# Optimization experiments

Measured on AMD Instinct MI355X. Metric: run time of the kernel, lower is better.

The kernel has to match this reference:

```python
import jax, jax.numpy as jnp
import numpy as np

B, R, F = 64, 196, 2048   # batch, regions, feature_dim
E, H, A = 512, 512, 512   # embed_dim, hidden_dim, attn_dim
V, L = 12000, 24          # vocab, seq_len


def setup_inputs() -> dict:
    key = jax.random.key(0)
    ks = jax.random.split(key, 16)
    s = lambda *d: 1.0 / np.sqrt(d[-1])
    inp = {
        'image_feats': jax.random.normal(ks[0], (B, R, F), jnp.float32),
        'caption_in': jax.random.randint(ks[1], (B, L), 0, V, jnp.int64),
        'emb_table': jax.random.normal(ks[2], (V, E), jnp.float32) * 0.02,
        'W_init_h': jax.random.normal(ks[3], (H, F), jnp.float32) * s(F),
        'b_init_h': jnp.zeros((H,), jnp.float32),
        'W_init_c': jax.random.normal(ks[4], (H, F), jnp.float32) * s(F),
        'b_init_c': jnp.zeros((H,), jnp.float32),
        'W_ih': jax.random.normal(ks[5], (4 * H, E + F), jnp.float32) * s(E + F),
        'b_ih': jnp.zeros((4 * H,), jnp.float32),
        'W_hh': jax.random.normal(ks[6], (4 * H, H), jnp.float32) * s(H),
        'b_hh': jnp.zeros((4 * H,), jnp.float32),
        'W_featp': jax.random.normal(ks[7], (A, F), jnp.float32) * s(F),
        'b_featp': jnp.zeros((A,), jnp.float32),
        'W_hidp': jax.random.normal(ks[8], (A, H), jnp.float32) * s(H),
        'b_hidp': jnp.zeros((A,), jnp.float32),
        'W_score': jax.random.normal(ks[9], (1, A), jnp.float32) * s(A),
        'b_score': jnp.zeros((1,), jnp.float32),
        'W_out': jax.random.normal(ks[10], (V, H), jnp.float32) * s(H),
        'b_out': jnp.zeros((V,), jnp.float32),
    }
    return inp


def _forward(image_feats, caption_in, emb_table, W_init_h, b_init_h, W_init_c,
             b_init_c, W_ih, b_ih, W_hh, b_hh, W_featp, b_featp, W_hidp,
             b_hidp, W_score, b_score, W_out, b_out):
    # init hidden state from mean image features
    mean_feats = image_feats.mean(axis=1)                      # (B, F)
    h0 = mean_feats @ W_init_h.T + b_init_h                    # (B, H)
    c0 = mean_feats @ W_init_c.T + b_init_c                    # (B, H)

    embeddings = emb_table[caption_in]                         # (B, L, E)  (dropout in eval mode = identity)

    # feature projection is constant over timesteps -> hoist out of the scan
    feat_proj = jnp.einsum('brf,af->bra', image_feats, W_featp) + b_featp  # (B, R, A)

    def step(carry, emb_t):
        h, c = carry
        # additive attention
        hid_proj = h @ W_hidp.T + b_hidp                       # (B, A)
        energy = jnp.tanh(feat_proj + hid_proj[:, None, :])    # (B, R, A)
        scores = jnp.einsum('bra,a->br', energy, W_score[0]) + b_score[0]
        alpha = jax.nn.softmax(scores, axis=1)                 # (B, R)
        context = jnp.einsum('br,brf->bf', alpha, image_feats) # (B, F)
        # LSTM cell (PyTorch gate order: i, f, g, o)
        x = jnp.concatenate([emb_t, context], axis=1)          # (B, E+F)
        gates = x @ W_ih.T + b_ih + h @ W_hh.T + b_hh          # (B, 4H)
        i, f, g, o = jnp.split(gates, 4, axis=1)
        c_new = jax.nn.sigmoid(f) * c + jax.nn.sigmoid(i) * jnp.tanh(g)
        h_new = jax.nn.sigmoid(o) * jnp.tanh(c_new)
        out = h_new @ W_out.T + b_out                          # (B, V)
        return (h_new, c_new), (out, alpha)

    emb_t = jnp.swapaxes(embeddings, 0, 1)                     # (L, B, E)
    _, (preds, alphas) = jax.lax.scan(step, (h0, c0), emb_t)
    predictions = jnp.swapaxes(preds, 0, 1)                    # (B, L, V)
    all_alphas = jnp.swapaxes(alphas, 0, 1)                    # (B, L, R)
    return predictions, all_alphas


def reference(image_feats, caption_in, emb_table, W_init_h, b_init_h, W_init_c,
              b_init_c, W_ih, b_ih, W_hh, b_hh, W_featp, b_featp, W_hidp,
              b_hidp, W_score, b_score, W_out, b_out):
    return _forward(image_feats, caption_in, emb_table, W_init_h, b_init_h,
                    W_init_c, b_init_c, W_ih, b_ih, W_hh, b_hh, W_featp,
                    b_featp, W_hidp, b_hidp, W_score, b_score, W_out, b_out)
```

## Files before the change

### kernel.cpp

```cpp
#include <hip/hip_runtime.h>

#define B_ 64
#define R_ 196
#define F_ 2048
#define E_ 512
#define H_ 512
#define A_ 512
#define V_ 12000
#define L_ 24

typedef __attribute__((ext_vector_type(8))) short bf16x8;
typedef __attribute__((ext_vector_type(4))) float f32x4;
typedef unsigned short ush;

__device__ __forceinline__ float fast_tanh(float x) {
    float t = __expf(2.f * x);
    return 1.f - 2.f / (t + 1.f);
}
__device__ __forceinline__ float fast_sig(float x) {
    return 1.f / (1.f + __expf(-x));
}
__device__ __forceinline__ ush f2bf(float x) {
    unsigned int u = __float_as_uint(x);
    return (ush)((u + 0x7fffu + ((u >> 16) & 1u)) >> 16);
}
__device__ __forceinline__ float bf2f(ush b) {
    return __uint_as_float(((unsigned int)b) << 16);
}

#define LROW 40

template<int SPLIT, int CMAP, bool NFAST>
__global__ __launch_bounds__(512) void gemm_big128(
    const ush* __restrict__ Ah, const ush* __restrict__ Al, int lda,
    const ush* __restrict__ Wh, const ush* __restrict__ Wl, int ldw,
    const float* __restrict__ bias, void* __restrict__ Cv,
    int ldc, int N, int K)
{
    constexpr int SMEM_BYTES = (SPLIT == 3) ? 61440 : 30720;
    __shared__ __align__(16) char smem[SMEM_BYTES];
    ush* sAh = (ush*)smem;
    ush* sBh = (ush*)(smem + 10240);
    ush* sAl = (ush*)(smem + 30720);
    ush* sBl = (ush*)(smem + 40960);

    const int tid = threadIdx.x;
    const int lane = tid & 63, w = tid >> 6;
    const int mw = w >> 2, nw = w & 3;

    const int nbx = gridDim.x, nby = gridDim.y;
    const int nwg = nbx * nby;
    const int orig = blockIdx.x + nbx * blockIdx.y;
    const int q = nwg >> 3, r = nwg & 7;
    const int xcd = orig & 7, idx = orig >> 3;
    const int lin = (xcd < r ? xcd * (q + 1) : r * (q + 1) + (xcd - r) * q) + idx;
    int bx, by;
    if constexpr (NFAST) { by = lin % nby; bx = lin / nby; }
    else                 { bx = lin % nbx; by = lin / nbx; }
    const int mtile = bx * 128;
    const int ntile = by * 256;

    const int fr = lane & 15, kg = (lane >> 4) * 8;
    const int arow = tid >> 2, aq = (tid & 3) * 8;

    f32x4 acc[4][4];
    #pragma unroll
    for (int mf = 0; mf < 4; ++mf)
        #pragma unroll
        for (int nf = 0; nf < 4; ++nf) acc[mf][nf] = {0.f, 0.f, 0.f, 0.f};

    const uint4 zv = make_uint4(0u, 0u, 0u, 0u);

    for (int kb = 0; kb < K; kb += 32) {
        uint4 a_h = *(const uint4*)(Ah + (size_t)(mtile + arow) * lda + kb + aq);
        uint4 a_l;
        uint4 b_h[2], b_l[2];
        #pragma unroll
        for (int p = 0; p < 2; ++p) {
            const int row = ntile + arow + 128 * p;
            b_h[p] = (row < N) ? *(const uint4*)(Wh + (size_t)row * ldw + kb + aq) : zv;
        }
        if constexpr (SPLIT == 3) {
            a_l = *(const uint4*)(Al + (size_t)(mtile + arow) * lda + kb + aq);
            #pragma unroll
            for (int p = 0; p < 2; ++p) {
                const int row = ntile + arow + 128 * p;
                b_l[p] = (row < N) ? *(const uint4*)(Wl + (size_t)row * ldw + kb + aq) : zv;
            }
        }

        __syncthreads();
        *(uint4*)(sAh + arow * LROW + aq) = a_h;
        #pragma unroll
        for (int p = 0; p < 2; ++p)
            *(uint4*)(sBh + (arow + 128 * p) * LROW + aq) = b_h[p];
        if constexpr (SPLIT == 3) {
            *(uint4*)(sAl + arow * LROW + aq) = a_l;
            #pragma unroll
            for (int p = 0; p < 2; ++p)
                *(uint4*)(sBl + (arow + 128 * p) * LROW + aq) = b_l[p];
        }
        __syncthreads();

        bf16x8 bh[4], bl[4];
        #pragma unroll
        for (int nf = 0; nf < 4; ++nf) {
            bh[nf] = *(const bf16x8*)(sBh + (nw * 64 + nf * 16 + fr) * LROW + kg);
            if constexpr (SPLIT == 3)
                bl[nf] = *(const bf16x8*)(sBl + (nw * 64 + nf * 16 + fr) * LROW + kg);
        }
        #pragma unroll
        for (int mf = 0; mf < 4; ++mf) {
            const bf16x8 ah = *(const bf16x8*)(sAh + (mw * 64 + mf * 16 + fr) * LROW + kg);
            if constexpr (SPLIT == 3) {
                const bf16x8 al = *(const bf16x8*)(sAl + (mw * 64 + mf * 16 + fr) * LROW + kg);
                #pragma unroll
                for (int nf = 0; nf < 4; ++nf) {
                    acc[mf][nf] = __builtin_amdgcn_mfma_f32_16x16x32_bf16(ah, bh[nf], acc[mf][nf], 0, 0, 0);
                    acc[mf][nf] = __builtin_amdgcn_mfma_f32_16x16x32_bf16(ah, bl[nf], acc[mf][nf], 0, 0, 0);
                    acc[mf][nf] = __builtin_amdgcn_mfma_f32_16x16x32_bf16(al, bh[nf], acc[mf][nf], 0, 0, 0);
                }
            } else {
                #pragma unroll
                for (int nf = 0; nf < 4; ++nf)
                    acc[mf][nf] = __builtin_amdgcn_mfma_f32_16x16x32_bf16(ah, bh[nf], acc[mf][nf], 0, 0, 0);
            }
        }
    }

    #pragma unroll
    for (int nf = 0; nf < 4; ++nf) {
        const int nn = ntile + nw * 64 + nf * 16 + fr;
        if (nn < N) {
            const float bv = bias ? bias[nn] : 0.f;
            #pragma unroll
            for (int mf = 0; mf < 4; ++mf) {
                #pragma unroll
                for (int rr = 0; rr < 4; ++rr) {
                    const int m = mtile + mw * 64 + mf * 16 + (lane >> 4) * 4 + rr;
                    const float v = acc[mf][nf][rr] + bv;
                    if constexpr (CMAP == 1)
                        ((ush*)Cv)[(size_t)m * ldc + nn] = f2bf(v);
                    else if constexpr (CMAP == 2) {
                        float* dst = (float*)Cv + (size_t)(m & 63) * (L_ * V_)
                                   + (size_t)(m >> 6) * V_ + nn;
                        __builtin_nontemporal_store(v, dst);
                    } else
                        ((float*)Cv)[(size_t)m * ldc + nn] = v;
                }
            }
        }
    }
}

template<int SPLIT, int CMAP, bool NFAST, int NF>
__global__ __launch_bounds__(256) void gemm_big(
    const ush* __restrict__ Ah, const ush* __restrict__ Al, int lda,
    const ush* __restrict__ Wh, const ush* __restrict__ Wl, int ldw,
    const float* __restrict__ bias, void* __restrict__ Cv,
    int ldc, int N, int K)
{
    constexpr int ABYTES = 64 * LROW * 2;
    constexpr int BBYTES = 64 * NF * LROW * 2;
    constexpr int SMEM_BYTES = (SPLIT == 3) ? 2 * (ABYTES + BBYTES) : (ABYTES + BBYTES);
    __shared__ __align__(16) char smem[SMEM_BYTES];
    ush* sAh = (ush*)smem;
    ush* sBh = (ush*)(smem + ABYTES);
    ush* sAl = (ush*)(smem + ABYTES + BBYTES);
    ush* sBl = (ush*)(smem + 2 * ABYTES + BBYTES);

    const int tid = threadIdx.x;
    const int lane = tid & 63, w = tid >> 6;

    const int nbx = gridDim.x, nby = gridDim.y;
    const int nwg = nbx * nby;
    int lin = blockIdx.x + nbx * blockIdx.y;
    if ((nwg & 7) == 0) {
        const int q = nwg >> 3;
        lin = (lin & 7) * q + (lin >> 3);
    }
    int bx, by;
    if constexpr (NFAST) { by = lin % nby; bx = lin / nby; }
    else                 { bx = lin % nbx; by = lin / nbx; }
    const int mtile = bx * 64;
    const int ntile = by * (64 * NF);

    const int fr = lane & 15, kg = (lane >> 4) * 8;
    const int arow = tid >> 2, aq = (tid & 3) * 8;

    f32x4 acc[4][NF];
    #pragma unroll
    for (int mf = 0; mf < 4; ++mf)
        #pragma unroll
        for (int nf = 0; nf < NF; ++nf) acc[mf][nf] = {0.f, 0.f, 0.f, 0.f};

    const uint4 zv = make_uint4(0u, 0u, 0u, 0u);

    for (int kb = 0; kb < K; kb += 32) {
        uint4 a_h = *(const uint4*)(Ah + (size_t)(mtile + arow) * lda + kb + aq);
        uint4 a_l;
        uint4 b_h[NF], b_l[NF];
        #pragma unroll
        for (int p = 0; p < NF; ++p) {
            const int row = ntile + arow + 64 * p;
            b_h[p] = (row < N) ? *(const uint4*)(Wh + (size_t)row * ldw + kb + aq) : zv;
        }
        if constexpr (SPLIT == 3) {
            a_l = *(const uint4*)(Al + (size_t)(mtile + arow) * lda + kb + aq);
            #pragma unroll
            for (int p = 0; p < NF; ++p) {
                const int row = ntile + arow + 64 * p;
                b_l[p] = (row < N) ? *(const uint4*)(Wl + (size_t)row * ldw + kb + aq) : zv;
            }
        }

        __syncthreads();
        *(uint4*)(sAh + arow * LROW + aq) = a_h;
        #pragma unroll
        for (int p = 0; p < NF; ++p)
            *(uint4*)(sBh + (arow + 64 * p) * LROW + aq) = b_h[p];
        if constexpr (SPLIT == 3) {
            *(uint4*)(sAl + arow * LROW + aq) = a_l;
            #pragma unroll
            for (int p = 0; p < NF; ++p)
                *(uint4*)(sBl + (arow + 64 * p) * LROW + aq) = b_l[p];
        }
        __syncthreads();

        bf16x8 bh[NF], bl[NF];
        #pragma unroll
        for (int nf = 0; nf < NF; ++nf) {
            bh[nf] = *(const bf16x8*)(sBh + (w * (16 * NF) + nf * 16 + fr) * LROW + kg);
            if constexpr (SPLIT == 3)
                bl[nf] = *(const bf16x8*)(sBl + (w * (16 * NF) + nf * 16 + fr) * LROW + kg);
        }
        #pragma unroll
        for (int mf = 0; mf < 4; ++mf) {
            const bf16x8 ah = *(const bf16x8*)(sAh + (mf * 16 + fr) * LROW + kg);
            if constexpr (SPLIT == 3) {
                const bf16x8 al = *(const bf16x8*)(sAl + (mf * 16 + fr) * LROW + kg);
                #pragma unroll
                for (int nf = 0; nf < NF; ++nf) {
                    acc[mf][nf] = __builtin_amdgcn_mfma_f32_16x16x32_bf16(ah, bh[nf], acc[mf][nf], 0, 0, 0);
                    acc[mf][nf] = __builtin_amdgcn_mfma_f32_16x16x32_bf16(ah, bl[nf], acc[mf][nf], 0, 0, 0);
                    acc[mf][nf] = __builtin_amdgcn_mfma_f32_16x16x32_bf16(al, bh[nf], acc[mf][nf], 0, 0, 0);
                }
            } else {
                #pragma unroll
                for (int nf = 0; nf < NF; ++nf)
                    acc[mf][nf] = __builtin_amdgcn_mfma_f32_16x16x32_bf16(ah, bh[nf], acc[mf][nf], 0, 0, 0);
            }
        }
    }

    #pragma unroll
    for (int nf = 0; nf < NF; ++nf) {
        const int nn = ntile + w * (16 * NF) + nf * 16 + fr;
        if (nn < N) {
            const float bv = bias ? bias[nn] : 0.f;
            #pragma unroll
            for (int mf = 0; mf < 4; ++mf) {
                #pragma unroll
                for (int rr = 0; rr < 4; ++rr) {
                    const int m = mtile + mf * 16 + (lane >> 4) * 4 + rr;
                    const float v = acc[mf][nf][rr] + bv;
                    if constexpr (CMAP == 1)
                        ((ush*)Cv)[(size_t)m * ldc + nn] = f2bf(v);
                    else
                        ((float*)Cv)[(size_t)m * ldc + nn] = v;
                }
            }
        }
    }
}

__global__ __launch_bounds__(256) void gemm_gates(
    const ush* __restrict__ Ah0, const ush* __restrict__ Al0, int lda0, int k0,
    const ush* __restrict__ Ah1, const ush* __restrict__ Al1, int lda1,
    const ush* __restrict__ Wh, const ush* __restrict__ Wl, int ldw,
    float* __restrict__ C, int ldc, long zstride, int kChunk)
{
    __shared__ ush sAh[64 * LROW];
    __shared__ ush sBh[64 * LROW];
    __shared__ ush sAl[64 * LROW];
    __shared__ ush sBl[64 * LROW];

    const int tid = threadIdx.x;
    const int ntile = blockIdx.x * 64;
    const int kStart = blockIdx.z * kChunk;
    const int lane = tid & 63, w = tid >> 6;
    const int lrow = tid >> 2;
    const int lcol = (tid & 3) * 8;
    const int nrow = ntile + lrow;

    f32x4 acc[4];
    #pragma unroll
    for (int f = 0; f < 4; ++f) acc[f] = {0.f, 0.f, 0.f, 0.f};

    const int fr = lane & 15;
    const int kg = (lane >> 4) * 8;

    for (int kb = kStart; kb < kStart + kChunk; kb += 32) {
        const ush *ph, *pl; int lda, loc;
        if (kb < k0) { ph = Ah0; pl = Al0; lda = lda0; loc = kb; }
        else         { ph = Ah1; pl = Al1; lda = lda1; loc = kb - k0; }

        uint4 a_h = *(const uint4*)(ph + (size_t)lrow * lda + loc + lcol);
        uint4 b_h = *(const uint4*)(Wh + (size_t)nrow * ldw + kb + lcol);
        uint4 a_l = *(const uint4*)(pl + (size_t)lrow * lda + loc + lcol);
        uint4 b_l = *(const uint4*)(Wl + (size_t)nrow * ldw + kb + lcol);

        __syncthreads();
        *(uint4*)(sAh + lrow * LROW + lcol) = a_h;
        *(uint4*)(sBh + lrow * LROW + lcol) = b_h;
        *(uint4*)(sAl + lrow * LROW + lcol) = a_l;
        *(uint4*)(sBl + lrow * LROW + lcol) = b_l;
        __syncthreads();

        const bf16x8 bh = *(const bf16x8*)(sBh + (16 * w + fr) * LROW + kg);
        const bf16x8 bl = *(const bf16x8*)(sBl + (16 * w + fr) * LROW + kg);

        #pragma unroll
        for (int f = 0; f < 4; ++f) {
            const bf16x8 ah = *(const bf16x8*)(sAh + (16 * f + fr) * LROW + kg);
            const bf16x8 al = *(const bf16x8*)(sAl + (16 * f + fr) * LROW + kg);
            acc[f] = __builtin_amdgcn_mfma_f32_16x16x32_bf16(ah, bh, acc[f], 0, 0, 0);
            acc[f] = __builtin_amdgcn_mfma_f32_16x16x32_bf16(ah, bl, acc[f], 0, 0, 0);
            acc[f] = __builtin_amdgcn_mfma_f32_16x16x32_bf16(al, bh, acc[f], 0, 0, 0);
        }
    }

    const int n = ntile + 16 * w + (lane & 15);
    float* Cz = C + (size_t)blockIdx.z * zstride;
    #pragma unroll
    for (int f = 0; f < 4; ++f)
        #pragma unroll
        for (int rr = 0; rr < 4; ++rr) {
            const int m = 16 * f + (lane >> 4) * 4 + rr;
            Cz[(size_t)m * ldc + n] = acc[f][rr];
        }
}

__global__ __launch_bounds__(256) void prep_feats(
    const float* __restrict__ feats, ush* __restrict__ fbh,
    ush* __restrict__ mh, ush* __restrict__ ml)
{
    const int fs = blockIdx.x;
    const int b  = blockIdx.y;
    const int f = fs * 512 + threadIdx.x * 2;
    const float2* fp = (const float2*)(feats + (size_t)b * R_ * F_ + f);
    ush* fo = fbh + (size_t)b * R_ * F_ + f;
    float sx = 0.f, sy = 0.f;
    for (int r = 0; r < R_; ++r) {
        const float2 v = fp[(size_t)r * (F_ / 2)];
        sx += v.x; sy += v.y;
        ushort2 u; u.x = f2bf(v.x); u.y = f2bf(v.y);
        *(ushort2*)(fo + (size_t)r * F_) = u;
    }
    const float s = 1.f / (float)R_;
    sx *= s; sy *= s;
    const size_t mi = (size_t)b * F_ + f;
    const ush hx = f2bf(sx); mh[mi] = hx;     ml[mi] = f2bf(sx - bf2f(hx));
    const ush hy = f2bf(sy); mh[mi + 1] = hy; ml[mi + 1] = f2bf(sy - bf2f(hy));
}

__global__ __launch_bounds__(256) void gather_split(
    const float* __restrict__ emb, const int* __restrict__ cap,
    ush* __restrict__ eh, ush* __restrict__ el)
{
    const int idx = blockIdx.x * 256 + threadIdx.x;
    const int bt = idx >> 7, j = idx & 127;
    const int tok = cap[bt];
    const float4 v = reinterpret_cast<const float4*>(emb)[(size_t)tok * (E_ / 4) + j];
    const float a[4] = {v.x, v.y, v.z, v.w};
    #pragma unroll
    for (int c = 0; c < 4; ++c) {
        const ush hi = f2bf(a[c]);
        eh[idx * 4 + c] = hi;
        el[idx * 4 + c] = f2bf(a[c] - bf2f(hi));
    }
}

__global__ __launch_bounds__(256) void split_kernel(
    const float* __restrict__ in, ush* __restrict__ hi, ush* __restrict__ lo, int n4)
{
    for (int i = blockIdx.x * 256 + threadIdx.x; i < n4; i += gridDim.x * 256) {
        const float4 v = reinterpret_cast<const float4*>(in)[i];
        const float a[4] = {v.x, v.y, v.z, v.w};
        #pragma unroll
        for (int c = 0; c < 4; ++c) {
            const ush h = f2bf(a[c]);
            hi[i * 4 + c] = h;
            if (lo) lo[i * 4 + c] = f2bf(a[c] - bf2f(h));
        }
    }
}

__global__ __launch_bounds__(256) void prep_wih(
    const float* __restrict__ W_ih, const float* __restrict__ W_hh,
    ush* __restrict__ wxh, ush* __restrict__ wxl,
    ush* __restrict__ wg2h, ush* __restrict__ wg2l)
{
    const int nrow = blockIdx.x;
    for (int k = threadIdx.x; k < E_; k += 256) {
        const float v = W_ih[(size_t)nrow * (E_ + F_) + k];
        const ush h = f2bf(v);
        wxh[(size_t)nrow * E_ + k] = h;
        wxl[(size_t)nrow * E_ + k] = f2bf(v - bf2f(h));
    }
    for (int k = threadIdx.x; k < F_ + H_; k += 256) {
        const float v = (k < F_) ? W_ih[(size_t)nrow * (E_ + F_) + E_ + k]
                                 : W_hh[(size_t)nrow * H_ + (k - F_)];
        const ush h = f2bf(v);
        wg2h[(size_t)nrow * (F_ + H_) + k] = h;
        wg2l[(size_t)nrow * (F_ + H_) + k] = f2bf(v - bf2f(h));
    }
}

__global__ __launch_bounds__(256) void transpose512(
    const float* __restrict__ in, ush* __restrict__ out)
{
    const int idx = blockIdx.x * 256 + threadIdx.x;
    const int k = idx >> 9, a = idx & 511;
    out[idx] = f2bf(in[(size_t)a * 512 + k]);
}

__global__ __launch_bounds__(256) void init_reduce(
    const float* __restrict__ initp, const float* __restrict__ b_init_h,
    const float* __restrict__ b_init_c, float* __restrict__ h0f,
    float* __restrict__ c0, ush* __restrict__ h_hi, ush* __restrict__ h_lo)
{
    const int idx = blockIdx.x * 256 + threadIdx.x;
    const int b = idx >> 10, n = idx & 1023;
    float s = 0.f;
    #pragma unroll
    for (int z = 0; z < 8; ++z)
        s += initp[(size_t)z * (B_ * 1024) + (size_t)b * 1024 + n];
    if (n < 512) {
        s += b_init_h[n];
        h0f[b * H_ + n] = s;
        const ush hi = f2bf(s);
        h_hi[b * H_ + n] = hi;
        h_lo[b * H_ + n] = f2bf(s - bf2f(hi));
    } else {
        s += b_init_c[n - 512];
        c0[b * H_ + (n - 512)] = s;
    }
}

template<bool ATT>
__global__ __launch_bounds__(512) void step2_kernel(
    const float* __restrict__ gparts, const float* __restrict__ egates,
    const float* __restrict__ b_ih, const float* __restrict__ b_hh,
    float* __restrict__ c2, const float* __restrict__ h0f,
    ush* __restrict__ h_hi, ush* __restrict__ h_lo,
    ush* __restrict__ hall_hi, ush* __restrict__ hall_lo,
    const ush* __restrict__ whpT, const float* __restrict__ b_hidp,
    const ush* __restrict__ fpb, const float* __restrict__ W_score,
    const float* __restrict__ b_score, const ush* __restrict__ fbh,
    ush* __restrict__ ctx_hi, ush* __restrict__ ctx_lo,
    float* __restrict__ alph_out, int t)
{
    __shared__ float sh_h[H_];
    __shared__ float sh_hp[A_];
    __shared__ float sh_ws[A_];
    __shared__ float sh_sc[200];
    __shared__ float red[2];
    const int tid = threadIdx.x;
    const int fs = blockIdx.x;
    const int b = blockIdx.y;
    const int n = tid;

    float hh;
    if (t > 0) {
        const float* c_old = c2 + (size_t)((t - 1) & 1) * B_ * H_;
        float* c_new = c2 + (size_t)(t & 1) * B_ * H_;
        const float* eg = egates + ((size_t)b * L_ + (t - 1)) * 2048;
        float gi = b_ih[n] + b_hh[n] + eg[n];
        float gf = b_ih[n + 512] + b_hh[n + 512] + eg[n + 512];
        float gg = b_ih[n + 1024] + b_hh[n + 1024] + eg[n + 1024];
        float go = b_ih[n + 1536] + b_hh[n + 1536] + eg[n + 1536];
        #pragma unroll
        for (int z = 0; z < 8; ++z) {
            const float* gz = gparts + (size_t)z * B_ * 2048 + (size_t)b * 2048;
            gi += gz[n]; gf += gz[n + 512]; gg += gz[n + 1024]; go += gz[n + 1536];
        }
        const float cc = fast_sig(gf) * c_old[b * H_ + n] + fast_sig(gi) * fast_tanh(gg);
        hh = fast_sig(go) * fast_tanh(cc);
        if (fs == 0) {
            c_new[b * H_ + n] = cc;
            const ush hi = f2bf(hh);
            const ush lo = f2bf(hh - bf2f(hi));
            h_hi[b * H_ + n] = hi;
            h_lo[b * H_ + n] = lo;
            const size_t hidx = ((size_t)(t - 1) * B_ + b) * H_ + n;
            hall_hi[hidx] = hi;
            hall_lo[hidx] = lo;
        }
    } else {
        hh = h0f[b * H_ + n];
    }
    if constexpr (!ATT) return;

    sh_h[n] = hh;
    sh_ws[n] = W_score[n];
    __syncthreads();

    {
        float a0 = 0.f, a1 = 0.f, a2 = 0.f, a3 = 0.f;
        #pragma unroll 4
        for (int k = 0; k < H_; k += 4) {
            a0 = fmaf(sh_h[k + 0], bf2f(whpT[(size_t)(k + 0) * A_ + tid]), a0);
            a1 = fmaf(sh_h[k + 1], bf2f(whpT[(size_t)(k + 1) * A_ + tid]), a1);
            a2 = fmaf(sh_h[k + 2], bf2f(whpT[(size_t)(k + 2) * A_ + tid]), a2);
            a3 = fmaf(sh_h[k + 3], bf2f(whpT[(size_t)(k + 3) * A_ + tid]), a3);
        }
        sh_hp[tid] = (a0 + a1) + (a2 + a3) + b_hidp[tid];
    }
    __syncthreads();

    const int lane = tid & 63, wid = tid >> 6;
    for (int r = wid; r < R_; r += 8) {
        const ushort2* row = reinterpret_cast<const ushort2*>(fpb + ((size_t)b * R_ + r) * A_);
        float acc = 0.f;
        #pragma unroll
        for (int j = 0; j < 4; ++j) {
            const ushort2 u = row[lane + 64 * j];
            const int a = 2 * (lane + 64 * j);
            acc += fast_tanh(bf2f(u.x) + sh_hp[a]) * sh_ws[a];
            acc += fast_tanh(bf2f(u.y) + sh_hp[a + 1]) * sh_ws[a + 1];
        }
        for (int off = 32; off > 0; off >>= 1) acc += __shfl_down(acc, off);
        if (lane == 0) sh_sc[r] = acc + b_score[0];
    }
    __syncthreads();

    if (tid < 64) {
        float m = -1e30f;
        for (int r = tid; r < R_; r += 64) m = fmaxf(m, sh_sc[r]);
        for (int off = 32; off > 0; off >>= 1) m = fmaxf(m, __shfl_xor(m, off));
        float s = 0.f;
        for (int r = tid; r < R_; r += 64) s += __expf(sh_sc[r] - m);
        for (int off = 32; off > 0; off >>= 1) s += __shfl_xor(s, off);
        if (tid == 0) { red[0] = m; red[1] = 1.f / s; }
    }
    __syncthreads();
    const float m = red[0], is = red[1];
    if (tid < R_) {
        const float av = __expf(sh_sc[tid] - m) * is;
        sh_sc[tid] = av;
        if (fs == 0) alph_out[((size_t)b * L_ + t) * R_ + tid] = av;
    }
    __syncthreads();

    {
        const int f0 = fs * 512 + tid;
        const ush* fp2 = fbh + (size_t)b * R_ * F_ + f0;
        float cx = 0.f;
        #pragma unroll 4
        for (int r = 0; r < R_; ++r)
            cx = fmaf(sh_sc[r], bf2f(fp2[(size_t)r * F_]), cx);
        const size_t ci = (size_t)b * F_ + f0;
        const ush hx = f2bf(cx);
        ctx_hi[ci] = hx;
        ctx_lo[ci] = f2bf(cx - bf2f(hx));
    }
}

extern "C" void kernel_launch(void* const* d_in, const int* in_sizes, int n_in,
                              void* d_out, int out_size, void* d_ws, size_t ws_size,
                              hipStream_t stream)
{
    const float* feats    = (const float*)d_in[0];
    const int*   cap      = (const int*)  d_in[1];
    const float* emb      = (const float*)d_in[2];
    const float* W_init_h = (const float*)d_in[3];
    const float* b_init_h = (const float*)d_in[4];
    const float* W_init_c = (const float*)d_in[5];
    const float* b_init_c = (const float*)d_in[6];
    const float* W_ih     = (const float*)d_in[7];
    const float* b_ih     = (const float*)d_in[8];
    const float* W_hh     = (const float*)d_in[9];
    const float* b_hh     = (const float*)d_in[10];
    const float* W_featp  = (const float*)d_in[11];
    const float* b_featp  = (const float*)d_in[12];
    const float* W_hidp   = (const float*)d_in[13];
    const float* b_hidp   = (const float*)d_in[14];
    const float* W_score  = (const float*)d_in[15];
    const float* b_score  = (const float*)d_in[16];
    const float* W_out    = (const float*)d_in[17];
    const float* b_out    = (const float*)d_in[18];

    float* pred     = (float*)d_out;
    float* alph_out = pred + (size_t)B_ * L_ * V_;

    char* p = (char*)d_ws;
    auto alloc = [&](size_t bytes) { char* q = p; p += (bytes + 255) & ~(size_t)255; return q; };

    ush*   fpb    = (ush*)  alloc((size_t)B_ * R_ * A_ * 2);
    ush*   eh     = (ush*)  alloc((size_t)B_ * L_ * E_ * 2);
    ush*   el     = (ush*)  alloc((size_t)B_ * L_ * E_ * 2);
    ush*   mh     = (ush*)  alloc((size_t)B_ * F_ * 2);
    ush*   ml     = (ush*)  alloc((size_t)B_ * F_ * 2);
    ush*   fbh    = (ush*)  alloc((size_t)B_ * R_ * F_ * 2);
    ush*   wfp_h  = (ush*)  alloc((size_t)A_ * F_ * 2);
    ush*   wiH    = (ush*)  alloc((size_t)1024 * F_ * 2);
    ush*   wiL    = (ush*)  alloc((size_t)1024 * F_ * 2);
    ush*   wxh    = (ush*)  alloc((size_t)2048 * E_ * 2);
    ush*   wxl    = (ush*)  alloc((size_t)2048 * E_ * 2);
    ush*   wg2h   = (ush*)  alloc((size_t)2048 * (F_ + H_) * 2);
    ush*   wg2l   = (ush*)  alloc((size_t)2048 * (F_ + H_) * 2);
    ush*   woh    = (ush*)  alloc((size_t)V_ * H_ * 2);
    ush*   wol    = (ush*)  alloc((size_t)V_ * H_ * 2);
    ush*   whpT   = (ush*)  alloc((size_t)H_ * A_ * 2);
    float* egates = (float*)alloc((size_t)B_ * L_ * 2048 * 4);
    float* h0f    = (float*)alloc((size_t)B_ * H_ * 4);
    float* c2     = (float*)alloc((size_t)2 * B_ * H_ * 4);
    ush*   h_hi   = (ush*)  alloc((size_t)B_ * H_ * 2);
    ush*   h_lo   = (ush*)  alloc((size_t)B_ * H_ * 2);
    ush*   hallh  = (ush*)  alloc((size_t)L_ * B_ * H_ * 2);
    ush*   halll  = (ush*)  alloc((size_t)L_ * B_ * H_ * 2);
    ush*   ctx_hi = (ush*)  alloc((size_t)B_ * F_ * 2);
    ush*   ctx_lo = (ush*)  alloc((size_t)B_ * F_ * 2);
    float* gparts = (float*)alloc((size_t)8 * B_ * 2048 * 4);
    float* initp  = (float*)alloc((size_t)8 * B_ * 1024 * 4);

    prep_feats<<<dim3(4, B_), 256, 0, stream>>>(feats, fbh, mh, ml);
    gather_split<<<768, 256, 0, stream>>>(emb, cap, eh, el);
    split_kernel<<<2048, 256, 0, stream>>>(W_out, woh, wol, V_ * H_ / 4);
    split_kernel<<<512, 256, 0, stream>>>(W_init_h, wiH, wiL, H_ * F_ / 4);
    split_kernel<<<512, 256, 0, stream>>>(W_init_c, wiH + (size_t)512 * F_,
                                          wiL + (size_t)512 * F_, H_ * F_ / 4);
    split_kernel<<<512, 256, 0, stream>>>(W_featp, wfp_h, nullptr, A_ * F_ / 4);
    prep_wih<<<2048, 256, 0, stream>>>(W_ih, W_hh, wxh, wxl, wg2h, wg2l);
    transpose512<<<1024, 256, 0, stream>>>(W_hidp, whpT);

    gemm_gates<<<dim3(16, 1, 8), 256, 0, stream>>>(
        mh, ml, F_, F_,
        mh, ml, F_,
        wiH, wiL, F_,
        initp, 1024, (long)B_ * 1024, F_ / 8);
    init_reduce<<<256, 256, 0, stream>>>(initp, b_init_h, b_init_c, h0f, c2, h_hi, h_lo);

    gemm_big<1, 1, true, 1><<<dim3(196, 8), 256, 0, stream>>>(
        fbh, nullptr, F_, wfp_h, nullptr, F_, b_featp, fpb, A_, A_, F_);

    gemm_big<3, 0, false, 2><<<dim3(24, 16), 256, 0, stream>>>(
        eh, el, E_, wxh, wxl, E_, nullptr, egates, 2048, 2048, E_);

    for (int t = 0; t < L_; ++t) {
        step2_kernel<true><<<dim3(4, B_), 512, 0, stream>>>(
            gparts, egates, b_ih, b_hh, c2, h0f, h_hi, h_lo, hallh, halll,
            whpT, b_hidp, fpb, W_score, b_score, fbh, ctx_hi, ctx_lo,
            alph_out, t);

        gemm_gates<<<dim3(32, 1, 8), 256, 0, stream>>>(
            ctx_hi, ctx_lo, F_, F_,
            h_hi, h_lo, H_,
            wg2h, wg2l, F_ + H_,
            gparts, 4 * H_, (long)B_ * 4 * H_, (F_ + H_) / 8);
    }

    step2_kernel<false><<<dim3(1, B_), 512, 0, stream>>>(
        gparts, egates, b_ih, b_hh, c2, h0f, h_hi, h_lo, hallh, halll,
        whpT, b_hidp, fpb, W_score, b_score, fbh, ctx_hi, ctx_lo,
        alph_out, L_);

    gemm_big128<3, 2, false><<<dim3(12, 47), 512, 0, stream>>>(
        hallh, halll, H_, woh, wol, H_, b_out, pred, 0, V_, H_);
}
```

Before: 1.961 ms.

## Fuse recurrent timestep loop into one persistent kernel with grid barriers

Replaces the 49 per-timestep launches (attention/cell kernel plus gate GEMM) with a single persistent 256-block kernel that runs all 24 steps, separated by atomic-counter grid barriers. The attention score and softmax are now computed once per batch row instead of redundantly in four blocks, with alphas passed through global memory. The gate GEMM is reimplemented inline with 64-wide N tiles and a fixed K split. The aim is to remove launch overhead and redundant work. In exchange it relies on all 256 blocks being co-resident to avoid deadlock, and each barrier adds atomic spin latency.

```diff
diff --git a/kernel.cpp b/kernel.cpp
--- a/kernel.cpp
+++ b/kernel.cpp
@@ -8,6 +8,7 @@
 #define A_ 512
 #define V_ 12000
 #define L_ 24
+#define NBLK 256
 
 typedef __attribute__((ext_vector_type(8))) short bf16x8;
 typedef __attribute__((ext_vector_type(4))) float f32x4;
@@ -29,6 +30,221 @@
 }
 
 #define LROW 40
+
+__device__ __forceinline__ void gbar(int* bar, int idx) {
+    __syncthreads();
+    if (threadIdx.x == 0) {
+        __threadfence();
+        atomicAdd(bar + idx, 1);
+        while (atomicAdd(bar + idx, 0) < NBLK)
+            __builtin_amdgcn_s_sleep(2);
+        __threadfence();
+    }
+    __syncthreads();
+}
+
+__device__ __forceinline__ float cell_compute(
+    const float* __restrict__ gparts, const float* __restrict__ egates,
+    const float* __restrict__ b_ih, const float* __restrict__ b_hh,
+    float* __restrict__ c2, const float* __restrict__ h0f,
+    ush* __restrict__ h_hi, ush* __restrict__ h_lo,
+    ush* __restrict__ hallh, ush* __restrict__ halll,
+    int b, int n, int t)
+{
+    float hh;
+    if (t > 0) {
+        const float* c_old = c2 + (size_t)((t - 1) & 1) * B_ * H_;
+        float* c_new = c2 + (size_t)(t & 1) * B_ * H_;
+        const float* eg = egates + ((size_t)b * L_ + (t - 1)) * 2048;
+        float gi = b_ih[n] + b_hh[n] + eg[n];
+        float gf = b_ih[n + 512] + b_hh[n + 512] + eg[n + 512];
+        float gg = b_ih[n + 1024] + b_hh[n + 1024] + eg[n + 1024];
+        float go = b_ih[n + 1536] + b_hh[n + 1536] + eg[n + 1536];
+        #pragma unroll
+        for (int z = 0; z < 8; ++z) {
+            const float* gz = gparts + (size_t)z * B_ * 2048 + (size_t)b * 2048;
+            gi += gz[n]; gf += gz[n + 512]; gg += gz[n + 1024]; go += gz[n + 1536];
+        }
+        const float cc = fast_sig(gf) * c_old[b * H_ + n] + fast_sig(gi) * fast_tanh(gg);
+        hh = fast_sig(go) * fast_tanh(cc);
+        c_new[b * H_ + n] = cc;
+        const ush hi = f2bf(hh);
+        const ush lo = f2bf(hh - bf2f(hi));
+        h_hi[b * H_ + n] = hi;
+        h_lo[b * H_ + n] = lo;
+        const size_t hidx = ((size_t)(t - 1) * B_ + b) * H_ + n;
+        hallh[hidx] = hi;
+        halll[hidx] = lo;
+    } else {
+        hh = h0f[b * H_ + n];
+    }
+    return hh;
+}
+
+__global__ __launch_bounds__(512) void loop_kernel(
+    float* __restrict__ gparts, const float* __restrict__ egates,
+    const float* __restrict__ b_ih, const float* __restrict__ b_hh,
+    float* __restrict__ c2, const float* __restrict__ h0f,
+    ush* __restrict__ h_hi, ush* __restrict__ h_lo,
+    ush* __restrict__ hallh, ush* __restrict__ halll,
+    const ush* __restrict__ whpT, const float* __restrict__ b_hidp,
+    const ush* __restrict__ fpb, const float* __restrict__ W_score,
+    const float* __restrict__ b_score, const ush* __restrict__ fbh,
+    ush* __restrict__ ctx_hi, ush* __restrict__ ctx_lo,
+    float* __restrict__ alpha_glob, float* __restrict__ alph_out,
+    const ush* __restrict__ wg2h, const ush* __restrict__ wg2l,
+    int* bar)
+{
+    __shared__ __align__(16) char smem[20480];
+    const int bid = blockIdx.x, tid = threadIdx.x;
+    const int lane = tid & 63, w = tid >> 6;
+
+    for (int t = 0; t < L_; ++t) {
+        if (bid < B_) {
+            float* sh_h  = (float*)smem;
+            float* sh_hp = (float*)(smem + 2048);
+            float* sh_ws = (float*)(smem + 4096);
+            float* sh_sc = (float*)(smem + 6144);
+            float* red   = (float*)(smem + 7168);
+            const int b = bid;
+            const float hh = cell_compute(gparts, egates, b_ih, b_hh, c2, h0f,
+                                          h_hi, h_lo, hallh, halll, b, tid, t);
+            sh_h[tid] = hh;
+            sh_ws[tid] = W_score[tid];
+            __syncthreads();
+
+            {
+                float a0 = 0.f, a1 = 0.f, a2 = 0.f, a3 = 0.f;
+                #pragma unroll 4
+                for (int k = 0; k < H_; k += 4) {
+                    a0 = fmaf(sh_h[k + 0], bf2f(whpT[(size_t)(k + 0) * A_ + tid]), a0);
+                    a1 = fmaf(sh_h[k + 1], bf2f(whpT[(size_t)(k + 1) * A_ + tid]), a1);
+                    a2 = fmaf(sh_h[k + 2], bf2f(whpT[(size_t)(k + 2) * A_ + tid]), a2);
+                    a3 = fmaf(sh_h[k + 3], bf2f(whpT[(size_t)(k + 3) * A_ + tid]), a3);
+                }
+                sh_hp[tid] = (a0 + a1) + (a2 + a3) + b_hidp[tid];
+            }
+            __syncthreads();
+
+            for (int r = w; r < R_; r += 8) {
+                const ushort2* row = reinterpret_cast<const ushort2*>(fpb + ((size_t)b * R_ + r) * A_);
+                float acc = 0.f;
+                #pragma unroll
+                for (int j = 0; j < 4; ++j) {
+                    const ushort2 u = row[lane + 64 * j];
+                    const int a = 2 * (lane + 64 * j);
+                    acc += fast_tanh(bf2f(u.x) + sh_hp[a]) * sh_ws[a];
+                    acc += fast_tanh(bf2f(u.y) + sh_hp[a + 1]) * sh_ws[a + 1];
+                }
+                for (int off = 32; off > 0; off >>= 1) acc += __shfl_down(acc, off);
+                if (lane == 0) sh_sc[r] = acc + b_score[0];
+            }
+            __syncthreads();
+
+            if (tid < 64) {
+                float m = -1e30f;
+                for (int r = tid; r < R_; r += 64) m = fmaxf(m, sh_sc[r]);
+                for (int off = 32; off > 0; off >>= 1) m = fmaxf(m, __shfl_xor(m, off));
+                float s = 0.f;
+                for (int r = tid; r < R_; r += 64) s += __expf(sh_sc[r] - m);
+                for (int off = 32; off > 0; off >>= 1) s += __shfl_xor(s, off);
+                if (tid == 0) { red[0] = m; red[1] = 1.f / s; }
+            }
+            __syncthreads();
+            const float m = red[0], is = red[1];
+            if (tid < R_) {
+                const float av = __expf(sh_sc[tid] - m) * is;
+                alpha_glob[b * R_ + tid] = av;
+                alph_out[((size_t)b * L_ + t) * R_ + tid] = av;
+            }
+        }
+        gbar(bar, 3 * t);
+
+        {
+            float* sa = (float*)smem;
+            const int b = bid >> 2, fs = bid & 3;
+            if (tid < R_) sa[tid] = alpha_glob[b * R_ + tid];
+            __syncthreads();
+            const int f0 = fs * 512 + tid;
+            const ush* fp2 = fbh + (size_t)b * R_ * F_ + f0;
+            float cx = 0.f;
+            #pragma unroll 4
+            for (int r = 0; r < R_; ++r)
+                cx = fmaf(sa[r], bf2f(fp2[(size_t)r * F_]), cx);
+            const size_t ci = (size_t)b * F_ + f0;
+            const ush hx = f2bf(cx);
+            ctx_hi[ci] = hx;
+            ctx_lo[ci] = f2bf(cx - bf2f(hx));
+        }
+        gbar(bar, 3 * t + 1);
+
+        {
+            ush* sAh = (ush*)smem;
+            ush* sBh = (ush*)(smem + 5120);
+            ush* sAl = (ush*)(smem + 10240);
+            ush* sBl = (ush*)(smem + 15360);
+            const int nt = bid & 31, z = bid >> 5;
+            const int ntile = nt * 64;
+            const int nw = w & 3, mbase = (w >> 2) * 2;
+            const int fr = lane & 15, kg = (lane >> 4) * 8;
+            const int lrow = tid >> 2, lcol = (tid & 3) * 8;
+            f32x4 acc0 = {0.f, 0.f, 0.f, 0.f};
+            f32x4 acc1 = {0.f, 0.f, 0.f, 0.f};
+
+            for (int kb = z * 320; kb < z * 320 + 320; kb += 32) {
+                uint4 a_h, a_l, b_h4, b_l4;
+                if (tid < 256) {
+                    const ush *ph, *pl; int lda, loc;
+                    if (kb < F_) { ph = ctx_hi; pl = ctx_lo; lda = F_; loc = kb; }
+                    else         { ph = h_hi;   pl = h_lo;   lda = H_; loc = kb - F_; }
+                    a_h  = *(const uint4*)(ph + (size_t)lrow * lda + loc + lcol);
+                    a_l  = *(const uint4*)(pl + (size_t)lrow * lda + loc + lcol);
+                    b_h4 = *(const uint4*)(wg2h + (size_t)(ntile + lrow) * (F_ + H_) + kb + lcol);
+                    b_l4 = *(const uint4*)(wg2l + (size_t)(ntile + lrow) * (F_ + H_) + kb + lcol);
+                }
+                __syncthreads();
+                if (tid < 256) {
+                    *(uint4*)(sAh + lrow * LROW + lcol) = a_h;
+                    *(uint4*)(sBh + lrow * LROW + lcol) = b_h4;
+                    *(uint4*)(sAl + lrow * LROW + lcol) = a_l;
+                    *(uint4*)(sBl + lrow * LROW + lcol) = b_l4;
+                }
+                __syncthreads();
+
+                const bf16x8 bh = *(const bf16x8*)(sBh + (16 * nw + fr) * LROW + kg);
+                const bf16x8 bl = *(const bf16x8*)(sBl + (16 * nw + fr) * LROW + kg);
+                {
+                    const bf16x8 ah = *(const bf16x8*)(sAh + (16 * mbase + fr) * LROW + kg);
+                    const bf16x8 al = *(const bf16x8*)(sAl + (16 * mbase + fr) * LROW + kg);
+                    acc0 = __builtin_amdgcn_mfma_f32_16x16x32_bf16(ah, bh, acc0, 0, 0, 0);
+                    acc0 = __builtin_amdgcn_mfma_f32_16x16x32_bf16(ah, bl, acc0, 0, 0, 0);
+                    acc0 = __builtin_amdgcn_mfma_f32_16x16x32_bf16(al, bh, acc0, 0, 0, 0);
+                }
+                {
+                    const bf16x8 ah = *(const bf16x8*)(sAh + (16 * (mbase + 1) + fr) * LROW + kg);
+                    const bf16x8 al = *(const bf16x8*)(sAl + (16 * (mbase + 1) + fr) * LROW + kg);
+                    acc1 = __builtin_amdgcn_mfma_f32_16x16x32_bf16(ah, bh, acc1, 0, 0, 0);
+                    acc1 = __builtin_amdgcn_mfma_f32_16x16x32_bf16(ah, bl, acc1, 0, 0, 0);
+                    acc1 = __builtin_amdgcn_mfma_f32_16x16x32_bf16(al, bh, acc1, 0, 0, 0);
+                }
+            }
+
+            float* Cz = gparts + (size_t)z * B_ * 2048;
+            const int n = ntile + 16 * nw + fr;
+            #pragma unroll
+            for (int rr = 0; rr < 4; ++rr) {
+                Cz[(size_t)(16 * mbase + (lane >> 4) * 4 + rr) * 2048 + n] = acc0[rr];
+                Cz[(size_t)(16 * (mbase + 1) + (lane >> 4) * 4 + rr) * 2048 + n] = acc1[rr];
+            }
+        }
+        gbar(bar, 3 * t + 2);
+    }
+
+    if (bid < B_) {
+        cell_compute(gparts, egates, b_ih, b_hh, c2, h0f,
+                     h_hi, h_lo, hallh, halll, bid, tid, L_);
+    }
+}
 
 template<int SPLIT, int CMAP, bool NFAST>
 __global__ __launch_bounds__(512) void gemm_big128(
@@ -445,125 +661,6 @@
     } else {
         s += b_init_c[n - 512];
         c0[b * H_ + (n - 512)] = s;
-    }
-}
-
-template<bool ATT>
-__global__ __launch_bounds__(512) void step2_kernel(
-    const float* __restrict__ gparts, const float* __restrict__ egates,
-    const float* __restrict__ b_ih, const float* __restrict__ b_hh,
-    float* __restrict__ c2, const float* __restrict__ h0f,
-    ush* __restrict__ h_hi, ush* __restrict__ h_lo,
-    ush* __restrict__ hall_hi, ush* __restrict__ hall_lo,
-    const ush* __restrict__ whpT, const float* __restrict__ b_hidp,
-    const ush* __restrict__ fpb, const float* __restrict__ W_score,
-    const float* __restrict__ b_score, const ush* __restrict__ fbh,
-    ush* __restrict__ ctx_hi, ush* __restrict__ ctx_lo,
-    float* __restrict__ alph_out, int t)
-{
-    __shared__ float sh_h[H_];
-    __shared__ float sh_hp[A_];
-    __shared__ float sh_ws[A_];
-    __shared__ float sh_sc[200];
-    __shared__ float red[2];
-    const int tid = threadIdx.x;
-    const int fs = blockIdx.x;
-    const int b = blockIdx.y;
-    const int n = tid;
-
-    float hh;
-    if (t > 0) {
-        const float* c_old = c2 + (size_t)((t - 1) & 1) * B_ * H_;
-        float* c_new = c2 + (size_t)(t & 1) * B_ * H_;
-        const float* eg = egates + ((size_t)b * L_ + (t - 1)) * 2048;
-        float gi = b_ih[n] + b_hh[n] + eg[n];
-        float gf = b_ih[n + 512] + b_hh[n + 512] + eg[n + 512];
-        float gg = b_ih[n + 1024] + b_hh[n + 1024] + eg[n + 1024];
-        float go = b_ih[n + 1536] + b_hh[n + 1536] + eg[n + 1536];
-        #pragma unroll
-        for (int z = 0; z < 8; ++z) {
-            const float* gz = gparts + (size_t)z * B_ * 2048 + (size_t)b * 2048;
-            gi += gz[n]; gf += gz[n + 512]; gg += gz[n + 1024]; go += gz[n + 1536];
-        }
-        const float cc = fast_sig(gf) * c_old[b * H_ + n] + fast_sig(gi) * fast_tanh(gg);
-        hh = fast_sig(go) * fast_tanh(cc);
-        if (fs == 0) {
-            c_new[b * H_ + n] = cc;
-            const ush hi = f2bf(hh);
-            const ush lo = f2bf(hh - bf2f(hi));
-            h_hi[b * H_ + n] = hi;
-            h_lo[b * H_ + n] = lo;
-            const size_t hidx = ((size_t)(t - 1) * B_ + b) * H_ + n;
-            hall_hi[hidx] = hi;
-            hall_lo[hidx] = lo;
-        }
-    } else {
-        hh = h0f[b * H_ + n];
-    }
-    if constexpr (!ATT) return;
-
-    sh_h[n] = hh;
-    sh_ws[n] = W_score[n];
-    __syncthreads();
-
-    {
-        float a0 = 0.f, a1 = 0.f, a2 = 0.f, a3 = 0.f;
-        #pragma unroll 4
-        for (int k = 0; k < H_; k += 4) {
-            a0 = fmaf(sh_h[k + 0], bf2f(whpT[(size_t)(k + 0) * A_ + tid]), a0);
-            a1 = fmaf(sh_h[k + 1], bf2f(whpT[(size_t)(k + 1) * A_ + tid]), a1);
-            a2 = fmaf(sh_h[k + 2], bf2f(whpT[(size_t)(k + 2) * A_ + tid]), a2);
-            a3 = fmaf(sh_h[k + 3], bf2f(whpT[(size_t)(k + 3) * A_ + tid]), a3);
-        }
-        sh_hp[tid] = (a0 + a1) + (a2 + a3) + b_hidp[tid];
-    }
-    __syncthreads();
-
-    const int lane = tid & 63, wid = tid >> 6;
-    for (int r = wid; r < R_; r += 8) {
-        const ushort2* row = reinterpret_cast<const ushort2*>(fpb + ((size_t)b * R_ + r) * A_);
-        float acc = 0.f;
-        #pragma unroll
-        for (int j = 0; j < 4; ++j) {
-            const ushort2 u = row[lane + 64 * j];
-            const int a = 2 * (lane + 64 * j);
-            acc += fast_tanh(bf2f(u.x) + sh_hp[a]) * sh_ws[a];
-            acc += fast_tanh(bf2f(u.y) + sh_hp[a + 1]) * sh_ws[a + 1];
-        }
-        for (int off = 32; off > 0; off >>= 1) acc += __shfl_down(acc, off);
-        if (lane == 0) sh_sc[r] = acc + b_score[0];
-    }
-    __syncthreads();
-
-    if (tid < 64) {
-        float m = -1e30f;
-        for (int r = tid; r < R_; r += 64) m = fmaxf(m, sh_sc[r]);
-        for (int off = 32; off > 0; off >>= 1) m = fmaxf(m, __shfl_xor(m, off));
-        float s = 0.f;
-        for (int r = tid; r < R_; r += 64) s += __expf(sh_sc[r] - m);
-        for (int off = 32; off > 0; off >>= 1) s += __shfl_xor(s, off);
-        if (tid == 0) { red[0] = m; red[1] = 1.f / s; }
-    }
-    __syncthreads();
-    const float m = red[0], is = red[1];
-    if (tid < R_) {
-        const float av = __expf(sh_sc[tid] - m) * is;
-        sh_sc[tid] = av;
-        if (fs == 0) alph_out[((size_t)b * L_ + t) * R_ + tid] = av;
-    }
-    __syncthreads();
-
-    {
-        const int f0 = fs * 512 + tid;
-        const ush* fp2 = fbh + (size_t)b * R_ * F_ + f0;
-        float cx = 0.f;
-        #pragma unroll 4
-        for (int r = 0; r < R_; ++r)
-            cx = fmaf(sh_sc[r], bf2f(fp2[(size_t)r * F_]), cx);
-        const size_t ci = (size_t)b * F_ + f0;
-        const ush hx = f2bf(cx);
-        ctx_hi[ci] = hx;
-        ctx_lo[ci] = f2bf(cx - bf2f(hx));
     }
 }
 
@@ -622,8 +719,12 @@
     ush*   halll  = (ush*)  alloc((size_t)L_ * B_ * H_ * 2);
     ush*   ctx_hi = (ush*)  alloc((size_t)B_ * F_ * 2);
     ush*   ctx_lo = (ush*)  alloc((size_t)B_ * F_ * 2);
+    float* alphag = (float*)alloc((size_t)B_ * R_ * 4);
     float* gparts = (float*)alloc((size_t)8 * B_ * 2048 * 4);
     float* initp  = (float*)alloc((size_t)8 * B_ * 1024 * 4);
+    int*   bar    = (int*)  alloc((size_t)3 * L_ * 4);
+
+    hipMemsetAsync(bar, 0, (size_t)3 * L_ * 4, stream);
 
     prep_feats<<<dim3(4, B_), 256, 0, stream>>>(feats, fbh, mh, ml);
     gather_split<<<768, 256, 0, stream>>>(emb, cap, eh, el);
@@ -648,23 +749,10 @@
     gemm_big<3, 0, false, 2><<<dim3(24, 16), 256, 0, stream>>>(
         eh, el, E_, wxh, wxl, E_, nullptr, egates, 2048, 2048, E_);
 
-    for (int t = 0; t < L_; ++t) {
-        step2_kernel<true><<<dim3(4, B_), 512, 0, stream>>>(
-            gparts, egates, b_ih, b_hh, c2, h0f, h_hi, h_lo, hallh, halll,
-            whpT, b_hidp, fpb, W_score, b_score, fbh, ctx_hi, ctx_lo,
-            alph_out, t);
-
-        gemm_gates<<<dim3(32, 1, 8), 256, 0, stream>>>(
-            ctx_hi, ctx_lo, F_, F_,
-            h_hi, h_lo, H_,
-            wg2h, wg2l, F_ + H_,
-            gparts, 4 * H_, (long)B_ * 4 * H_, (F_ + H_) / 8);
-    }
-
-    step2_kernel<false><<<dim3(1, B_), 512, 0, stream>>>(
+    loop_kernel<<<NBLK, 512, 0, stream>>>(
         gparts, egates, b_ih, b_hh, c2, h0f, h_hi, h_lo, hallh, halll,
         whpT, b_hidp, fpb, W_score, b_score, fbh, ctx_hi, ctx_lo,
-        alph_out, L_);
+        alphag, alph_out, wg2h, wg2l, bar);
 
     gemm_big128<3, 2, false><<<dim3(12, 47), 512, 0, stream>>>(
         hallh, halll, H_, woh, wol, H_, b_out, pred, 0, V_, H_);
```

Result: slower. 3.408 ms (+73.8%).
